# Optimization experiments

Measured on AMD Instinct MI355X. Metric: run time of the kernel, lower is better.

Reference implementation:

```python
import jax, jax.numpy as jnp
import numpy as np

B, F, C, H, W = 16, 256, 64, 64, 64   # batch, features, z_channels(e_dim), height, width
N_E = 512                              # codebooksize
BETA = 1.0
EPS = 1e-5


def setup_inputs() -> dict:
    key = jax.random.key(0)
    ks = jax.random.split(key, 4)
    x = jax.random.normal(ks[0], (B, F, H, W), jnp.float32)
    emb = jax.random.normal(ks[1], (N_E, C), jnp.float32)
    emb = emb / jnp.linalg.norm(emb, axis=1, keepdims=True)  # points on hypersphere
    return dict(
        x=x,
        bn1_gamma=jnp.ones((F,), jnp.float32),
        bn1_beta=jnp.zeros((F,), jnp.float32),
        conv1_w=jax.random.normal(ks[2], (C, F), jnp.float32) * np.float32(1.0 / np.sqrt(F)),
        conv1_b=jnp.zeros((C,), jnp.float32),
        conv2_w=jax.random.normal(ks[3], (C, C), jnp.float32) * np.float32(1.0 / np.sqrt(C)),
        conv2_b=jnp.zeros((C,), jnp.float32),
        embedding=emb,
        r=jnp.ones((N_E,), jnp.float32),
    )


def reference(x, bn1_gamma, bn1_beta, conv1_w, conv1_b, conv2_w, conv2_b, embedding, r):
    sg = jax.lax.stop_gradient
    # BatchNorm2d (training mode: batch stats, biased variance)
    mu = x.mean(axis=(0, 2, 3), keepdims=True)
    var = x.var(axis=(0, 2, 3), keepdims=True)
    x1 = (x - mu) * jax.lax.rsqrt(var + EPS)
    x1 = x1 * bn1_gamma[None, :, None, None] + bn1_beta[None, :, None, None]
    # 1x1 convs (note: original overwrites norm2 output, conv2 consumes conv1 output directly)
    x1 = jnp.einsum('bfhw,cf->bchw', x1, conv1_w) + conv1_b[None, :, None, None]
    z = jnp.einsum('bchw,oc->bohw', x1, conv2_w) + conv2_b[None, :, None, None]

    zf = z.reshape(-1, C)  # [B*C*H*W/e_dim view == flat rows of e_dim]
    # codebook angular statistics (norms detached, as torch.Tensor(list) detaches)
    d1 = embedding @ embedding.T                                 # [n_e, n_e]
    en = sg(jnp.linalg.norm(embedding, axis=1))                  # [n_e]
    edx = jnp.clip(d1 / (en[:, None] * en[None, :]), -0.99999, 0.99999)
    ang = jnp.arccos(edx)
    total_min_distance = jnp.mean(jnp.sort(ang, axis=0)[1])      # kthvalue(.,2,dim=0)
    codebookvariance = jnp.mean(jnp.var(ang, axis=1, ddof=1))    # torch.var unbiased

    # VQ dispatch: squared L2 distances + argmin + gather
    d = (zf ** 2).sum(1, keepdims=True) + (embedding ** 2).sum(1) - 2.0 * (zf @ embedding.T)
    idx = jnp.argmin(d, axis=1)                                  # [ntok]
    z_q = embedding[idx].reshape(z.shape)

    hsw = jnp.mean(jnp.square(r - en))
    # legacy=True path with beta=1.0, ignorezq=False, disentangle=True
    loss = jnp.mean((sg(z_q) - z) ** 2) + BETA * jnp.mean((z_q - sg(z)) ** 2)
    loss = loss + hsw + (codebookvariance - total_min_distance)

    z_q = z + sg(z_q - z)  # straight-through
    cb_loss = jnp.float32(0.0)  # prev_cb is None
    r_c = r + sg(jnp.clip(r, 0.9, 1.1) - r)  # Clamp with straight-through grad
    mean_r = jnp.mean(r_c)
    return (loss, z_q, codebookvariance, total_min_distance, hsw, cb_loss, mean_r)
```

## Files before the change

kernel.cpp:

```cpp
#include <hip/hip_runtime.h>
#include <math.h>


#define CAP    2048
#define MARGIN 4e-3f

#define WS_WHI  0
#define WS_WLO  8192
#define WS_BP   16384
#define WS_EN   16448
#define WS_E2   16960
#define WS_ACC  17472
#define WS_CNT  17480
#define WS_WL   17488
#define WS_EFT  19536
#define WS_WD   52304
#define WS_BPD  85072
#define WS_EHI  85200
#define WS_ELO  101584
#define WS_PART 117968
#define WS_SV   122064
#define WS_SM   122576

typedef __attribute__((ext_vector_type(8))) __bf16 bf16v8;
typedef __attribute__((ext_vector_type(2))) __bf16 bf16v2;
typedef __attribute__((ext_vector_type(4))) float  f32v4;
typedef __attribute__((ext_vector_type(4))) unsigned u32v4;

__device__ __forceinline__ unsigned short f2bf(float f) {
    __bf16 h = (__bf16)f;
    return __builtin_bit_cast(unsigned short, h);
}
__device__ __forceinline__ float bf2f(unsigned short h) {
    union { unsigned u; float f; } v; v.u = ((unsigned)h) << 16; return v.f;
}
__device__ __forceinline__ unsigned pack_bf2(float a, float b) {
    bf16v2 v = { (__bf16)a, (__bf16)b };
    return __builtin_bit_cast(unsigned, v);
}
__device__ __forceinline__ float bfhi(float a) {
    return (float)(__bf16)a;
}
__device__ __forceinline__ void load_lds16(const float* g, unsigned* l) {
    __builtin_amdgcn_global_load_lds((const __attribute__((address_space(1))) void*)g,
                                     (__attribute__((address_space(3))) void*)l, 16, 0, 0);
}

__global__ __launch_bounds__(256) void bn_stats_prep(
    const float* __restrict__ x, double* __restrict__ part,
    const float* __restrict__ emb,
    float* __restrict__ eft, float* __restrict__ en, float* __restrict__ e2,
    unsigned short* __restrict__ ehi, unsigned short* __restrict__ elo,
    float* __restrict__ sv, float* __restrict__ sm)
{
    const int t = threadIdx.x;

    if (blockIdx.x < 1024) {
        const int f = blockIdx.x >> 2, ch = blockIdx.x & 3;
        double s0 = 0.0, s1 = 0.0, q0 = 0.0, q1 = 0.0, q2 = 0.0, q3 = 0.0;
        #pragma unroll
        for (int bb = 0; bb < 4; ++bb) {
            const int b = ch * 4 + bb;
            const float4* p = (const float4*)(x + ((size_t)(b * 256 + f) << 12));
            #pragma unroll
            for (int ii = 0; ii < 4; ++ii) {
                float4 u = p[t + ii * 256];
                double dx = u.x, dy = u.y, dz = u.z, dw = u.w;
                s0 += dx + dy; s1 += dz + dw;
                q0 = fma(dx, dx, q0); q1 = fma(dy, dy, q1);
                q2 = fma(dz, dz, q2); q3 = fma(dw, dw, q3);
            }
        }
        double s = s0 + s1, q = (q0 + q1) + (q2 + q3);
        #pragma unroll
        for (int off = 32; off; off >>= 1) { s += __shfl_xor(s, off, 64); q += __shfl_xor(q, off, 64); }
        __shared__ double sh[8];
        const int wv = t >> 6;
        if ((t & 63) == 0) { sh[wv * 2] = s; sh[wv * 2 + 1] = q; }
        __syncthreads();
        if (t == 0) {
            part[blockIdx.x * 2]     = (sh[0] + sh[2]) + (sh[4] + sh[6]);
            part[blockIdx.x * 2 + 1] = (sh[1] + sh[3]) + (sh[5] + sh[7]);
        }
    } else if (blockIdx.x < 1088) {
        const int blk = blockIdx.x - 1024;
        const int lane = t & 63, wv = t >> 6;
        #pragma unroll
        for (int rr = 0; rr < 2; ++rr) {
            int n = blk * 8 + rr * 4 + wv;
            float v = emb[n * 64 + lane];
            eft[lane * 512 + n] = v;
            unsigned short hb = f2bf(v);
            unsigned short lb = f2bf(v - bf2f(hb));
            int pos = (lane >> 3) ^ (n & 7);
            ehi[n * 64 + pos * 8 + (lane & 7)] = hb;
            elo[n * 64 + pos * 8 + (lane & 7)] = lb;
            float qq = v * v;
            #pragma unroll
            for (int off = 32; off; off >>= 1) qq += __shfl_xor(qq, off, 64);
            if (lane == 0) { e2[n] = qq; en[n] = sqrtf(qq); }
        }
    } else {
        const int i = blockIdx.x - 1088;
        const int lane = t & 63, wv = t >> 6;
        __shared__ float ei_sh[64];
        __shared__ float ang[512];
        if (t < 64) ei_sh[t] = emb[(i << 6) + t];
        __syncthreads();
        float ni0 = 0.f, ni1 = 0.f, ni2 = 0.f, ni3 = 0.f;
        #pragma unroll
        for (int k = 0; k < 64; k += 4) {
            ni0 = fmaf(ei_sh[k + 0], ei_sh[k + 0], ni0);
            ni1 = fmaf(ei_sh[k + 1], ei_sh[k + 1], ni1);
            ni2 = fmaf(ei_sh[k + 2], ei_sh[k + 2], ni2);
            ni3 = fmaf(ei_sh[k + 3], ei_sh[k + 3], ni3);
        }
        const float eni = sqrtf((ni0 + ni1) + (ni2 + ni3));
        #pragma unroll
        for (int jj = 0; jj < 2; ++jj) {
            const int j = t + jj * 256;
            const float4* er = (const float4*)(emb + ((size_t)j << 6));
            float d0 = 0.f, d1 = 0.f, d2 = 0.f, d3 = 0.f;
            float n0 = 0.f, n1 = 0.f, n2 = 0.f, n3 = 0.f;
            #pragma unroll
            for (int k4 = 0; k4 < 16; ++k4) {
                float4 u = er[k4];
                const float* e4 = ei_sh + k4 * 4;
                d0 = fmaf(u.x, e4[0], d0); d1 = fmaf(u.y, e4[1], d1);
                d2 = fmaf(u.z, e4[2], d2); d3 = fmaf(u.w, e4[3], d3);
                n0 = fmaf(u.x, u.x, n0);   n1 = fmaf(u.y, u.y, n1);
                n2 = fmaf(u.z, u.z, n2);   n3 = fmaf(u.w, u.w, n3);
            }
            float dot = (d0 + d1) + (d2 + d3);
            float enj = sqrtf((n0 + n1) + (n2 + n3));
            float xv = dot / (eni * enj);
            xv = fminf(fmaxf(xv, -0.99999f), 0.99999f);
            ang[j] = acosf(xv);
        }
        __syncthreads();
        if (wv == 0) {
            float m1 = 3.4e38f, m2 = 3.4e38f, ssum = 0.f;
            #pragma unroll
            for (int t8 = 0; t8 < 8; ++t8) {
                float a = ang[t8 * 64 + lane];
                ssum += a;
                if (a < m1) { m2 = m1; m1 = a; }
                else if (a < m2) m2 = a;
            }
            #pragma unroll
            for (int off = 32; off; off >>= 1) ssum += __shfl_xor(ssum, off, 64);
            #pragma unroll
            for (int off = 32; off; off >>= 1) {
                float o1 = __shfl_xor(m1, off, 64);
                float o2 = __shfl_xor(m2, off, 64);
                if (o1 < m1) { m2 = fminf(m1, o2); m1 = o1; }
                else          m2 = fminf(m2, o1);
            }
            float mean = ssum * (1.f / 512.f);
            float vs = 0.f;
            #pragma unroll
            for (int t8 = 0; t8 < 8; ++t8) {
                float tt = ang[t8 * 64 + lane] - mean;
                vs = fmaf(tt, tt, vs);
            }
            #pragma unroll
            for (int off = 32; off; off >>= 1) vs += __shfl_xor(vs, off, 64);
            if (lane == 0) { sv[i] = vs * (1.f / 511.f); sm[i] = m2; }
        }
    }
}

__global__ __launch_bounds__(256) void prep(
    const float* __restrict__ w1, const float* __restrict__ w2,
    const float* __restrict__ b1, const float* __restrict__ b2,
    const float* __restrict__ gamma, const float* __restrict__ beta,
    const double* __restrict__ part,
    unsigned short* __restrict__ whi, unsigned short* __restrict__ wlo,
    double* __restrict__ Wd,
    double* __restrict__ bpd, float* __restrict__ bp,
    float* __restrict__ accs, int* __restrict__ cnt)
{
    __shared__ double sh_ad[4];
    __shared__ double cdl[256];
    __shared__ double red[4][64];
    __shared__ double tsh[64];
    const int t = threadIdx.x;

    if (blockIdx.x < 64) {
        const int o = t & 63, fi = t >> 6;
        const int f = blockIdx.x * 4 + fi;
        if (o == 0) {
            double s = (part[(4 * f) * 2]     + part[(4 * f + 1) * 2])
                     + (part[(4 * f + 2) * 2] + part[(4 * f + 3) * 2]);
            double q = (part[(4 * f) * 2 + 1]     + part[(4 * f + 1) * 2 + 1])
                     + (part[(4 * f + 2) * 2 + 1] + part[(4 * f + 3) * 2 + 1]);
            double mean = s * (1.0 / 65536.0);
            double var  = q * (1.0 / 65536.0) - mean * mean;
            sh_ad[fi] = (double)gamma[f] / sqrt(var + 1e-5);
        }
        __syncthreads();
        double s = 0.0;
        for (int c = 0; c < 64; ++c)
            s = fma((double)w2[o * 64 + c], (double)w1[c * 256 + f], s);
        double wp = s * sh_ad[fi];
        Wd[o * 256 + f] = wp;
        {
            float wpf = (float)wp;
            unsigned short wh = f2bf(wpf);
            unsigned short wlv = f2bf(wpf - bf2f(wh));
            int mt = o >> 4, cq_ = o & 15, sK = f >> 5, qd_ = (f >> 3) & 3, j = f & 7;
            int idx = ((mt * 8 + sK) * 64 + qd_ * 16 + cq_) * 8 + j;
            whi[idx] = wh; wlo[idx] = wlv;
        }
    } else {
        {
            const int f = t;
            double s = (part[(4 * f) * 2]     + part[(4 * f + 1) * 2])
                     + (part[(4 * f + 2) * 2] + part[(4 * f + 3) * 2]);
            double q = (part[(4 * f) * 2 + 1]     + part[(4 * f + 1) * 2 + 1])
                     + (part[(4 * f + 2) * 2 + 1] + part[(4 * f + 3) * 2 + 1]);
            double mean = s * (1.0 / 65536.0);
            double var  = q * (1.0 / 65536.0) - mean * mean;
            double a = (double)gamma[f] / sqrt(var + 1e-5);
            cdl[f] = (double)beta[f] - mean * a;
        }
        __syncthreads();
        const int o = t & 63, p = t >> 6;
        double ss = 0.0;
        for (int j = 0; j < 64; ++j) {
            int fidx = p * 64 + j;
            ss = fma((double)w1[o * 256 + fidx], cdl[fidx], ss);
        }
        red[p][o] = ss; __syncthreads();
        if (t < 64) tsh[t] = (double)b1[t] + (red[0][t] + red[1][t]) + (red[2][t] + red[3][t]);
        __syncthreads();
        if (t < 64) {
            double bb = (double)b2[t];
            for (int c = 0; c < 64; ++c)
                bb = fma((double)w2[t * 64 + c], tsh[c], bb);
            bpd[t] = bb;
            bp[t]  = (float)bb;
        }
        if (t < 8) accs[t] = 0.f;
        if (t == 0) cnt[0] = 0;
    }
}

__global__ __launch_bounds__(256, 2) void fused_gemm_vq(
    const float* __restrict__ x,
    const unsigned short* __restrict__ whi,
    const unsigned short* __restrict__ wlo,
    const float* __restrict__ bp,
    const float* __restrict__ emb,
    const float* __restrict__ e2,
    const unsigned short* __restrict__ ehi,
    const unsigned short* __restrict__ elo,
    float* __restrict__ accs,
    int* __restrict__ cnt, int* __restrict__ wl,
    float* __restrict__ zq)
{
    __shared__ __align__(16) unsigned smem[4880];
    enum { OAR = 0,
           OE2 = 4096, OZ2 = 4608, ODT = 4672, OD2T = 4736, OIT = 4800 };
    float* e2s = (float*)(smem + OE2);
    float* z2s = (float*)(smem + OZ2);
    float* dT  = (float*)(smem + ODT);
    float* d2T = (float*)(smem + OD2T);
    int*   iT  = (int*)(smem + OIT);

    const int tid = threadIdx.x, lane = tid & 63, wv = tid >> 6;
    const int wvu = __builtin_amdgcn_readfirstlane(wv);
    const int b = blockIdx.x >> 6, h = blockIdx.x & 63;
    const int cq = lane & 15, qd = lane >> 4;

    bf16v8 Ahi[8], Alo[8];
    #pragma unroll
    for (int s = 0; s < 8; ++s) {
        Ahi[s] = *(const bf16v8*)(whi + ((size_t)((wvu * 8 + s) * 64 + lane)) * 8);
        Alo[s] = *(const bf16v8*)(wlo + ((size_t)((wvu * 8 + s) * 64 + lane)) * 8);
    }
    float bpv[4];
    #pragma unroll
    for (int r = 0; r < 4; ++r) bpv[r] = bp[wvu * 16 + qd * 4 + r];
    e2s[tid]       = e2[tid];
    e2s[tid + 256] = e2[tid + 256];

    const float* xb = x + ((size_t)(b * 256 + wvu * 16) << 12) + (h << 6) + lane;
    float xva[16], xvb[16];
    #pragma unroll
    for (int i = 0; i < 16; ++i) xva[i] = xb[(size_t)i << 12];
    #pragma unroll
    for (int i = 0; i < 16; ++i) xvb[i] = xb[((size_t)(64 + i)) << 12];

    f32v4 acc[4];
    #pragma unroll
    for (int nt = 0; nt < 4; ++nt) acc[nt] = (f32v4){bpv[0], bpv[1], bpv[2], bpv[3]};

#define GEMM_CHUNK(CHK, CUR)                                                          \
    {                                                                                 \
        __syncthreads();                                                 \
        {                                                                             \
            unsigned hb[8], lb[8];                                                    \
            _Pragma("unroll")                                                         \
            for (int p = 0; p < 8; ++p) {                                             \
                float a = CUR[2 * p], bq = CUR[2 * p + 1];                            \
                hb[p] = pack_bf2(a, bq);                                              \
                lb[p] = pack_bf2(a - bfhi(a), bq - bfhi(bq));                         \
            }                                                                         \
            const int b0 = lane * 32 + (((2 * wvu) ^ (lane & 7)) << 2);               \
            const int b1 = lane * 32 + (((2 * wvu + 1) ^ (lane & 7)) << 2);           \
            *(u32v4*)(smem + OAR + b0)        = (u32v4){hb[0], hb[1], hb[2], hb[3]};  \
            *(u32v4*)(smem + OAR + b1)        = (u32v4){hb[4], hb[5], hb[6], hb[7]};  \
            *(u32v4*)(smem + OAR + 2048 + b0) = (u32v4){lb[0], lb[1], lb[2], lb[3]};  \
            *(u32v4*)(smem + OAR + 2048 + b1) = (u32v4){lb[4], lb[5], lb[6], lb[7]};  \
        }                                                                             \
        __syncthreads();                                                \
        if (CHK < 2) {                               \
            const float* xb2 = xb + ((size_t)((CHK + 2) * 64) << 12);                 \
            _Pragma("unroll")                                                         \
            for (int i = 0; i < 16; ++i) CUR[i] = xb2[(size_t)i << 12];               \
        }                                                                             \
        _Pragma("unroll")                                                             \
        for (int st2 = 0; st2 < 2; ++st2) {                                           \
            const int s = CHK * 2 + st2;                                              \
            _Pragma("unroll")                                                         \
            for (int nt = 0; nt < 4; ++nt) {                                          \
                const int row = nt * 16 + cq;                                         \
                const int pos = row * 32 + (((st2 * 4 + qd) ^ (row & 7)) << 2);       \
                bf16v8 bh = *(const bf16v8*)(smem + OAR + pos);                       \
                bf16v8 bl = *(const bf16v8*)(smem + OAR + 2048 + pos);                \
                acc[nt] = __builtin_amdgcn_mfma_f32_16x16x32_bf16(Ahi[s], bh, acc[nt], 0, 0, 0); \
                acc[nt] = __builtin_amdgcn_mfma_f32_16x16x32_bf16(Ahi[s], bl, acc[nt], 0, 0, 0); \
                acc[nt] = __builtin_amdgcn_mfma_f32_16x16x32_bf16(Alo[s], bh, acc[nt], 0, 0, 0); \
            }                                                                         \
        }                                                                             \
    }

    GEMM_CHUNK(0, xva)
    GEMM_CHUNK(1, xvb)
    GEMM_CHUNK(2, xva)
    GEMM_CHUNK(3, xvb)
#undef GEMM_CHUNK

    __syncthreads();

    {
        float z2p[4];
        #pragma unroll
        for (int r = 0; r < 4; ++r) {
            float p2 = 0.f;
            #pragma unroll
            for (int nt = 0; nt < 4; ++nt) p2 = fmaf(acc[nt][r], acc[nt][r], p2);
            #pragma unroll
            for (int off = 1; off <= 8; off <<= 1) p2 += __shfl_xor(p2, off, 64);
            z2p[r] = p2;
        }
        if (cq == 0) {
            #pragma unroll
            for (int r = 0; r < 4; ++r) z2s[wvu * 16 + qd * 4 + r] = z2p[r];
        }
        unsigned short* ar = (unsigned short*)(smem + OAR);
        #pragma unroll
        for (int nt = 0; nt < 4; ++nt) {
            const int w = nt * 16 + cq;
            const int gz = w >> 3, kj = w & 7;
            #pragma unroll
            for (int r = 0; r < 4; ++r) {
                const int tok = wvu * 16 + qd * 4 + r;
                const int hw = tok * 64 + ((gz ^ (tok & 7)) << 3) + kj;
                unsigned short zh = f2bf(acc[nt][r]);
                ar[hw]        = zh;
                ar[4096 + hw] = f2bf(acc[nt][r] - bf2f(zh));
            }
        }
    }
    __syncthreads();

    const int x7 = cq & 7;
    bf16v8 vahi[2], valo[2];
    {
        const int rbase = (wvu * 16 + cq) * 32;
        #pragma unroll
        for (int s = 0; s < 2; ++s) {
            int pos = ((s * 4 + qd) ^ x7) * 4;
            vahi[s] = *(const bf16v8*)(smem + OAR + rbase + pos);
            valo[s] = *(const bf16v8*)(smem + OAR + 2048 + rbase + pos);
        }
    }
    __syncthreads();

    {
        const float* gh = (const float*)ehi;
        const float* gl = (const float*)elo;
        load_lds16(gh + wvu * 256 + lane * 4,        smem + OAR + wvu * 256);
        load_lds16(gl + wvu * 256 + lane * 4,        smem + OAR + 1024 + wvu * 256);
        load_lds16(gh + 1024 + wvu * 256 + lane * 4, smem + OAR + 2048 + wvu * 256);
        load_lds16(gl + 1024 + wvu * 256 + lane * 4, smem + OAR + 3072 + wvu * 256);
    }

    float m1[4] = {-3.4e38f, -3.4e38f, -3.4e38f, -3.4e38f};
    float m2[4] = {-3.4e38f, -3.4e38f, -3.4e38f, -3.4e38f};
    int   i1[4] = {0, 0, 0, 0};
    const int p0 = (qd ^ x7) * 4, p1 = ((4 + qd) ^ x7) * 4;

    #pragma unroll 1
    for (int t2 = 0; t2 < 32; ++t2) {
        if ((t2 & 1) == 0) {
            __syncthreads();
            int st = t2 >> 1;
            if (st >= 1 && st < 15) {
                const float* gh = (const float*)ehi + (size_t)(st + 1) * 1024;
                const float* gl = (const float*)elo + (size_t)(st + 1) * 1024;
                unsigned* dst = smem + OAR + ((st + 1) & 1) * 2048;
                load_lds16(gh + wvu * 256 + lane * 4, dst + wvu * 256);
                load_lds16(gl + wvu * 256 + lane * 4, dst + 1024 + wvu * 256);
            }
        }
        const int rb = OAR + ((t2 >> 1) & 1) * 2048 + ((t2 & 1) * 16 + cq) * 32;
        bf16v8 bh0 = *(const bf16v8*)(smem + rb + p0);
        bf16v8 bh1 = *(const bf16v8*)(smem + rb + p1);
        bf16v8 bl0 = *(const bf16v8*)(smem + rb + 1024 + p0);
        bf16v8 bl1 = *(const bf16v8*)(smem + rb + 1024 + p1);
        const float eps = e2s[t2 * 16 + cq];
        f32v4 a = {0.f, 0.f, 0.f, 0.f};
        __builtin_amdgcn_s_setprio(1);
        a = __builtin_amdgcn_mfma_f32_16x16x32_bf16(vahi[0], bh0, a, 0, 0, 0);
        a = __builtin_amdgcn_mfma_f32_16x16x32_bf16(vahi[1], bh1, a, 0, 0, 0);
        a = __builtin_amdgcn_mfma_f32_16x16x32_bf16(vahi[0], bl0, a, 0, 0, 0);
        a = __builtin_amdgcn_mfma_f32_16x16x32_bf16(vahi[1], bl1, a, 0, 0, 0);
        a = __builtin_amdgcn_mfma_f32_16x16x32_bf16(valo[0], bh0, a, 0, 0, 0);
        a = __builtin_amdgcn_mfma_f32_16x16x32_bf16(valo[1], bh1, a, 0, 0, 0);
        __builtin_amdgcn_s_setprio(0);
        const int n = t2 * 16 + cq;
        #pragma unroll
        for (int r = 0; r < 4; ++r) {
            float s = fmaf(-0.5f, eps, a[r]);
            bool gt = s > m1[r];
            m2[r] = fminf(fmaxf(s, m2[r]), m1[r]);
            i1[r] = gt ? n : i1[r];
            m1[r] = fmaxf(s, m1[r]);
        }
    }

    #pragma unroll
    for (int r = 0; r < 4; ++r) {
        #pragma unroll
        for (int off = 1; off <= 8; off <<= 1) {
            float o1 = __shfl_xor(m1[r], off, 64);
            float o2 = __shfl_xor(m2[r], off, 64);
            int   oi = __shfl_xor(i1[r], off, 64);
            if (o1 > m1[r] || (o1 == m1[r] && oi < i1[r])) {
                m2[r] = fmaxf(m1[r], o2); m1[r] = o1; i1[r] = oi;
            } else {
                m2[r] = fmaxf(m2[r], o1);
            }
        }
    }
    if (cq == 0) {
        #pragma unroll
        for (int r = 0; r < 4; ++r) {
            int tok = wvu * 16 + qd * 4 + r;
            dT[tok] = m1[r]; d2T[tok] = m2[r]; iT[tok] = i1[r];
        }
    }
    __syncthreads();

    if (wv == 0) {
        float s1 = dT[lane], s2 = d2T[lane];
        if (s1 - s2 < MARGIN * 0.5f) {
            int pos = atomicAdd(cnt, 1);
            if (pos < CAP) wl[pos] = ((b << 6) + lane) * 64 + h;
        }
        float ms = z2s[lane] - 2.f * s1;
        #pragma unroll
        for (int off = 32; off; off >>= 1) ms += __shfl_xor(ms, off, 64);
        if (lane == 0) atomicAdd(accs + 0, ms);
    }
    __syncthreads();

    float* zrow = zq + ((size_t)(b * 64) << 12) + (h << 6) + lane;
    #pragma unroll
    for (int cc = 0; cc < 16; ++cc) {
        int c = wvu * 16 + cc;
        int id = iT[c];
        zrow[(size_t)c << 12] = emb[(id << 6) + lane];
    }
}

__global__ __launch_bounds__(256) void refine_fin(
    const float* __restrict__ x,
    const double* __restrict__ Wd,
    const double* __restrict__ bpd,
    const float* __restrict__ emb,
    const float* __restrict__ eft,
    const int* __restrict__ cnt, const int* __restrict__ wl,
    float* __restrict__ zq,
    const float* __restrict__ accs, const float* __restrict__ en,
    const float* __restrict__ sv, const float* __restrict__ sm,
    const float* __restrict__ r, float* __restrict__ out)
{
    const int tid = threadIdx.x, lane = tid & 63, wv = tid >> 6;

    if (blockIdx.x == 2048) {
        if (wv == 0) {
            float hs = 0.f, rs = 0.f, cv = 0.f, tm = 0.f;
            #pragma unroll
            for (int jj = 0; jj < 8; ++jj) {
                int n = (jj << 6) + lane;
                float rv = r[n];
                float d = rv - en[n];
                hs = fmaf(d, d, hs);
                rs += fminf(fmaxf(rv, 0.9f), 1.1f);
                cv += sv[n];
                tm += sm[n];
            }
            #pragma unroll
            for (int off = 32; off; off >>= 1) {
                hs += __shfl_xor(hs, off, 64); rs += __shfl_xor(rs, off, 64);
                cv += __shfl_xor(cv, off, 64); tm += __shfl_xor(tm, off, 64);
            }
            if (lane == 0) {
                float hsw    = hs * (1.f / 512.f);
                float mean_r = rs * (1.f / 512.f);
                float mse    = accs[0] * (1.f / 4194304.f);
                float cbv    = cv * (1.f / 512.f);
                float tmd    = tm * (1.f / 512.f);
                float loss   = 2.f * mse + hsw + (cbv - tmd);
                out[0]       = loss;
                out[4194305] = cbv;
                out[4194306] = tmd;
                out[4194307] = hsw;
                out[4194308] = 0.f;
                out[4194309] = mean_r;
            }
        }
        return;
    }

    int count = cnt[0]; if (count > CAP) count = CAP;
    const int it = blockIdx.x;
    if (it >= count) return;

    __shared__ double zp[4][64];
    __shared__ double zs[64];
    __shared__ double dsh[4];
    __shared__ int    ish[4];

    const int r2 = wl[it];
    const int b = r2 >> 12, c = (r2 >> 6) & 63, h = r2 & 63;

    {
        const float* xp = x + (((size_t)(b * 256 + wv * 64)) << 12) + (h << 6) + lane;
        const double* wrow = Wd + c * 256 + wv * 64;
        double zc0 = 0.0, zc1 = 0.0, zc2 = 0.0, zc3 = 0.0;
        double zc4 = 0.0, zc5 = 0.0, zc6 = 0.0, zc7 = 0.0;
        #pragma unroll
        for (int f = 0; f < 64; f += 8) {
            float a0 = xp[(size_t)(f + 0) << 12];
            float a1 = xp[(size_t)(f + 1) << 12];
            float a2 = xp[(size_t)(f + 2) << 12];
            float a3 = xp[(size_t)(f + 3) << 12];
            float a4 = xp[(size_t)(f + 4) << 12];
            float a5 = xp[(size_t)(f + 5) << 12];
            float a6 = xp[(size_t)(f + 6) << 12];
            float a7 = xp[(size_t)(f + 7) << 12];
            zc0 = fma(wrow[f + 0], (double)a0, zc0);
            zc1 = fma(wrow[f + 1], (double)a1, zc1);
            zc2 = fma(wrow[f + 2], (double)a2, zc2);
            zc3 = fma(wrow[f + 3], (double)a3, zc3);
            zc4 = fma(wrow[f + 4], (double)a4, zc4);
            zc5 = fma(wrow[f + 5], (double)a5, zc5);
            zc6 = fma(wrow[f + 6], (double)a6, zc6);
            zc7 = fma(wrow[f + 7], (double)a7, zc7);
        }
        zp[wv][lane] = ((zc0 + zc1) + (zc2 + zc3)) + ((zc4 + zc5) + (zc6 + zc7));
    }
    __syncthreads();
    if (tid < 64) zs[tid] = (zp[0][tid] + zp[1][tid]) + (zp[2][tid] + zp[3][tid]) + bpd[c];
    __syncthreads();

    const int n0 = tid, n1 = tid + 256;
    double d0a = 0.0, d0b = 0.0, d0c = 0.0, d0d = 0.0;
    double d1a = 0.0, d1b = 0.0, d1c = 0.0, d1d = 0.0;
    #pragma unroll 4
    for (int k = 0; k < 64; k += 4) {
        double z0 = zs[k], z1 = zs[k + 1], z2 = zs[k + 2], z3 = zs[k + 3];
        double t;
        t = z0 - (double)eft[((k + 0) << 9) + n0]; d0a = fma(t, t, d0a);
        t = z1 - (double)eft[((k + 1) << 9) + n0]; d0b = fma(t, t, d0b);
        t = z2 - (double)eft[((k + 2) << 9) + n0]; d0c = fma(t, t, d0c);
        t = z3 - (double)eft[((k + 3) << 9) + n0]; d0d = fma(t, t, d0d);
        t = z0 - (double)eft[((k + 0) << 9) + n1]; d1a = fma(t, t, d1a);
        t = z1 - (double)eft[((k + 1) << 9) + n1]; d1b = fma(t, t, d1b);
        t = z2 - (double)eft[((k + 2) << 9) + n1]; d1c = fma(t, t, d1c);
        t = z3 - (double)eft[((k + 3) << 9) + n1]; d1d = fma(t, t, d1d);
    }
    double d0 = (d0a + d0b) + (d0c + d0d);
    double d1 = (d1a + d1b) + (d1c + d1d);
    double dm; int im;
    if (d1 < d0) { dm = d1; im = n1; } else { dm = d0; im = n0; }

    #pragma unroll
    for (int off = 32; off; off >>= 1) {
        double od = __shfl_xor(dm, off, 64);
        int    oi = __shfl_xor(im, off, 64);
        if (od < dm || (od == dm && oi < im)) { dm = od; im = oi; }
    }
    if (lane == 0) { dsh[wv] = dm; ish[wv] = im; }
    __syncthreads();

    if (tid < 64) {
        double best = dsh[0]; int bi = ish[0];
        #pragma unroll
        for (int wq = 1; wq < 4; ++wq) {
            double od = dsh[wq]; int oi = ish[wq];
            if (od < best || (od == best && oi < bi)) { best = od; bi = oi; }
        }
        zq[((size_t)r2 << 6) + tid] = emb[(bi << 6) + tid];
    }
}

extern "C" void kernel_launch(void* const* d_in, const int* in_sizes, int n_in,
                              void* d_out, int out_size, void* d_ws, size_t ws_size,
                              hipStream_t stream) {
    const float* x   = (const float*)d_in[0];
    const float* g1  = (const float*)d_in[1];
    const float* be1 = (const float*)d_in[2];
    const float* w1  = (const float*)d_in[3];
    const float* b1  = (const float*)d_in[4];
    const float* w2  = (const float*)d_in[5];
    const float* b2  = (const float*)d_in[6];
    const float* emb = (const float*)d_in[7];
    const float* r   = (const float*)d_in[8];
    float* ws = (float*)d_ws;
    float* out = (float*)d_out;

    double* WD   = (double*)(ws + WS_WD);
    double* BPD  = (double*)(ws + WS_BPD);
    double* PART = (double*)(ws + WS_PART);
    int*    CNT  = (int*)(ws + WS_CNT);
    int*    WL   = (int*)(ws + WS_WL);
    unsigned short* WHI = (unsigned short*)(ws + WS_WHI);
    unsigned short* WLO = (unsigned short*)(ws + WS_WLO);
    unsigned short* EHI = (unsigned short*)(ws + WS_EHI);
    unsigned short* ELO = (unsigned short*)(ws + WS_ELO);

    bn_stats_prep<<<1600, 256, 0, stream>>>(x, PART, emb,
                                            ws + WS_EFT, ws + WS_EN, ws + WS_E2,
                                            EHI, ELO, ws + WS_SV, ws + WS_SM);
    prep<<<65, 256, 0, stream>>>(w1, w2, b1, b2, g1, be1, PART,
                                 WHI, WLO, WD, BPD, ws + WS_BP,
                                 ws + WS_ACC, CNT);
    fused_gemm_vq<<<1024, 256, 0, stream>>>(x, WHI, WLO, ws + WS_BP,
                                            emb, ws + WS_E2,
                                            EHI, ELO, ws + WS_ACC, CNT, WL, out + 1);
    refine_fin<<<2049, 256, 0, stream>>>(x, WD, BPD, emb, ws + WS_EFT, CNT, WL,
                                         out + 1, ws + WS_ACC, ws + WS_EN,
                                         ws + WS_SV, ws + WS_SM, r, out);
}
```

Baseline: 183.8 us.

## Fuse four kernels into one persistent kernel with global barriers

```diff
diff --git a/kernel.cpp b/kernel.cpp
--- a/kernel.cpp
+++ b/kernel.cpp
@@ -4,6 +4,7 @@
 
 #define CAP    2048
 #define MARGIN 4e-3f
+#define NBLK   512
 
 #define WS_WHI  0
 #define WS_WLO  8192
@@ -21,6 +22,7 @@
 #define WS_PART 117968
 #define WS_SV   122064
 #define WS_SM   122576
+#define WS_BAR  123088
 
 typedef __attribute__((ext_vector_type(8))) __bf16 bf16v8;
 typedef __attribute__((ext_vector_type(2))) __bf16 bf16v2;
@@ -46,21 +48,43 @@
                                      (__attribute__((address_space(3))) void*)l, 16, 0, 0);
 }
 
-__global__ __launch_bounds__(256) void bn_stats_prep(
-    const float* __restrict__ x, double* __restrict__ part,
-    const float* __restrict__ emb,
-    float* __restrict__ eft, float* __restrict__ en, float* __restrict__ e2,
+__device__ __forceinline__ void gbar(int* bar, int target) {
+    __syncthreads();
+    if (threadIdx.x == 0) {
+        __threadfence();
+        atomicAdd(bar, 1);
+        while (__hip_atomic_load(bar, __ATOMIC_RELAXED, __HIP_MEMORY_SCOPE_AGENT) < target)
+            __builtin_amdgcn_s_sleep(2);
+        __threadfence();
+    }
+    __syncthreads();
+}
+
+__global__ __launch_bounds__(256, 2) void mega(
+    const float* __restrict__ x,
+    const float* __restrict__ w1, const float* __restrict__ w2,
+    const float* __restrict__ b1, const float* __restrict__ b2,
+    const float* __restrict__ gamma, const float* __restrict__ beta,
+    const float* __restrict__ emb, const float* __restrict__ r,
+    unsigned short* __restrict__ whi, unsigned short* __restrict__ wlo,
+    float* __restrict__ bp, float* __restrict__ en, float* __restrict__ e2,
+    float* __restrict__ accs, int* __restrict__ cnt, int* __restrict__ wl,
+    float* __restrict__ eft, double* __restrict__ Wd, double* __restrict__ bpd,
+    double* __restrict__ part,
     unsigned short* __restrict__ ehi, unsigned short* __restrict__ elo,
-    float* __restrict__ sv, float* __restrict__ sm)
+    float* __restrict__ sv, float* __restrict__ sm,
+    int* __restrict__ bar, float* __restrict__ out, float* __restrict__ zq)
 {
-    const int t = threadIdx.x;
-
-    if (blockIdx.x < 1024) {
-        const int f = blockIdx.x >> 2, ch = blockIdx.x & 3;
+    __shared__ __align__(16) unsigned smem[4880];
+    const int t = threadIdx.x, lane = t & 63, wv = t >> 6;
+    const int bid = blockIdx.x;
+
+    {
+        const int f = bid >> 1, ch = bid & 1;
         double s0 = 0.0, s1 = 0.0, q0 = 0.0, q1 = 0.0, q2 = 0.0, q3 = 0.0;
-        #pragma unroll
-        for (int bb = 0; bb < 4; ++bb) {
-            const int b = ch * 4 + bb;
+        #pragma unroll 2
+        for (int bb = 0; bb < 8; ++bb) {
+            const int b = ch * 8 + bb;
             const float4* p = (const float4*)(x + ((size_t)(b * 256 + f) << 12));
             #pragma unroll
             for (int ii = 0; ii < 4; ++ii) {
@@ -74,165 +98,142 @@
         double s = s0 + s1, q = (q0 + q1) + (q2 + q3);
         #pragma unroll
         for (int off = 32; off; off >>= 1) { s += __shfl_xor(s, off, 64); q += __shfl_xor(q, off, 64); }
-        __shared__ double sh[8];
-        const int wv = t >> 6;
-        if ((t & 63) == 0) { sh[wv * 2] = s; sh[wv * 2 + 1] = q; }
+        double* shd = (double*)smem;
+        if (lane == 0) { shd[wv * 2] = s; shd[wv * 2 + 1] = q; }
         __syncthreads();
         if (t == 0) {
-            part[blockIdx.x * 2]     = (sh[0] + sh[2]) + (sh[4] + sh[6]);
-            part[blockIdx.x * 2 + 1] = (sh[1] + sh[3]) + (sh[5] + sh[7]);
-        }
-    } else if (blockIdx.x < 1088) {
-        const int blk = blockIdx.x - 1024;
-        const int lane = t & 63, wv = t >> 6;
-        #pragma unroll
-        for (int rr = 0; rr < 2; ++rr) {
-            int n = blk * 8 + rr * 4 + wv;
-            float v = emb[n * 64 + lane];
-            eft[lane * 512 + n] = v;
-            unsigned short hb = f2bf(v);
-            unsigned short lb = f2bf(v - bf2f(hb));
-            int pos = (lane >> 3) ^ (n & 7);
-            ehi[n * 64 + pos * 8 + (lane & 7)] = hb;
-            elo[n * 64 + pos * 8 + (lane & 7)] = lb;
-            float qq = v * v;
-            #pragma unroll
-            for (int off = 32; off; off >>= 1) qq += __shfl_xor(qq, off, 64);
-            if (lane == 0) { e2[n] = qq; en[n] = sqrtf(qq); }
-        }
-    } else {
-        const int i = blockIdx.x - 1088;
-        const int lane = t & 63, wv = t >> 6;
-        __shared__ float ei_sh[64];
-        __shared__ float ang[512];
-        if (t < 64) ei_sh[t] = emb[(i << 6) + t];
-        __syncthreads();
-        float ni0 = 0.f, ni1 = 0.f, ni2 = 0.f, ni3 = 0.f;
-        #pragma unroll
-        for (int k = 0; k < 64; k += 4) {
-            ni0 = fmaf(ei_sh[k + 0], ei_sh[k + 0], ni0);
-            ni1 = fmaf(ei_sh[k + 1], ei_sh[k + 1], ni1);
-            ni2 = fmaf(ei_sh[k + 2], ei_sh[k + 2], ni2);
-            ni3 = fmaf(ei_sh[k + 3], ei_sh[k + 3], ni3);
-        }
-        const float eni = sqrtf((ni0 + ni1) + (ni2 + ni3));
-        #pragma unroll
-        for (int jj = 0; jj < 2; ++jj) {
-            const int j = t + jj * 256;
-            const float4* er = (const float4*)(emb + ((size_t)j << 6));
-            float d0 = 0.f, d1 = 0.f, d2 = 0.f, d3 = 0.f;
-            float n0 = 0.f, n1 = 0.f, n2 = 0.f, n3 = 0.f;
-            #pragma unroll
-            for (int k4 = 0; k4 < 16; ++k4) {
-                float4 u = er[k4];
-                const float* e4 = ei_sh + k4 * 4;
-                d0 = fmaf(u.x, e4[0], d0); d1 = fmaf(u.y, e4[1], d1);
-                d2 = fmaf(u.z, e4[2], d2); d3 = fmaf(u.w, e4[3], d3);
-                n0 = fmaf(u.x, u.x, n0);   n1 = fmaf(u.y, u.y, n1);
-                n2 = fmaf(u.z, u.z, n2);   n3 = fmaf(u.w, u.w, n3);
-            }
-            float dot = (d0 + d1) + (d2 + d3);
-            float enj = sqrtf((n0 + n1) + (n2 + n3));
-            float xv = dot / (eni * enj);
-            xv = fminf(fmaxf(xv, -0.99999f), 0.99999f);
-            ang[j] = acosf(xv);
-        }
-        __syncthreads();
-        if (wv == 0) {
-            float m1 = 3.4e38f, m2 = 3.4e38f, ssum = 0.f;
-            #pragma unroll
-            for (int t8 = 0; t8 < 8; ++t8) {
-                float a = ang[t8 * 64 + lane];
-                ssum += a;
-                if (a < m1) { m2 = m1; m1 = a; }
-                else if (a < m2) m2 = a;
-            }
-            #pragma unroll
-            for (int off = 32; off; off >>= 1) ssum += __shfl_xor(ssum, off, 64);
-            #pragma unroll
-            for (int off = 32; off; off >>= 1) {
-                float o1 = __shfl_xor(m1, off, 64);
-                float o2 = __shfl_xor(m2, off, 64);
-                if (o1 < m1) { m2 = fminf(m1, o2); m1 = o1; }
-                else          m2 = fminf(m2, o1);
-            }
-            float mean = ssum * (1.f / 512.f);
-            float vs = 0.f;
-            #pragma unroll
-            for (int t8 = 0; t8 < 8; ++t8) {
-                float tt = ang[t8 * 64 + lane] - mean;
-                vs = fmaf(tt, tt, vs);
-            }
-            #pragma unroll
-            for (int off = 32; off; off >>= 1) vs += __shfl_xor(vs, off, 64);
-            if (lane == 0) { sv[i] = vs * (1.f / 511.f); sm[i] = m2; }
+            part[bid * 2]     = (shd[0] + shd[2]) + (shd[4] + shd[6]);
+            part[bid * 2 + 1] = (shd[1] + shd[3]) + (shd[5] + shd[7]);
+        }
+
+        if (bid >= 448) {
+            const int blk = bid - 448;
+            #pragma unroll
+            for (int rr = 0; rr < 2; ++rr) {
+                int n = blk * 8 + rr * 4 + wv;
+                float v = emb[n * 64 + lane];
+                eft[lane * 512 + n] = v;
+                unsigned short hb = f2bf(v);
+                unsigned short lb = f2bf(v - bf2f(hb));
+                int pos = (lane >> 3) ^ (n & 7);
+                ehi[n * 64 + pos * 8 + (lane & 7)] = hb;
+                elo[n * 64 + pos * 8 + (lane & 7)] = lb;
+                float qq = v * v;
+                #pragma unroll
+                for (int off = 32; off; off >>= 1) qq += __shfl_xor(qq, off, 64);
+                if (lane == 0) { e2[n] = qq; en[n] = sqrtf(qq); }
+            }
+        }
+
+        {
+            const int i = bid;
+            float* ei_sh = (float*)(smem + 64);
+            float* ang   = (float*)(smem + 128);
+            if (t < 64) ei_sh[t] = emb[(i << 6) + t];
+            __syncthreads();
+            float ni0 = 0.f, ni1 = 0.f, ni2 = 0.f, ni3 = 0.f;
+            #pragma unroll
+            for (int k = 0; k < 64; k += 4) {
+                ni0 = fmaf(ei_sh[k + 0], ei_sh[k + 0], ni0);
+                ni1 = fmaf(ei_sh[k + 1], ei_sh[k + 1], ni1);
+                ni2 = fmaf(ei_sh[k + 2], ei_sh[k + 2], ni2);
+                ni3 = fmaf(ei_sh[k + 3], ei_sh[k + 3], ni3);
+            }
+            const float eni = sqrtf((ni0 + ni1) + (ni2 + ni3));
+            #pragma unroll
+            for (int jj = 0; jj < 2; ++jj) {
+                const int j = t + jj * 256;
+                const float4* er = (const float4*)(emb + ((size_t)j << 6));
+                float d0 = 0.f, d1 = 0.f, d2 = 0.f, d3 = 0.f;
+                float n0 = 0.f, n1 = 0.f, n2 = 0.f, n3 = 0.f;
+                #pragma unroll
+                for (int k4 = 0; k4 < 16; ++k4) {
+                    float4 u = er[k4];
+                    const float* e4 = ei_sh + k4 * 4;
+                    d0 = fmaf(u.x, e4[0], d0); d1 = fmaf(u.y, e4[1], d1);
+                    d2 = fmaf(u.z, e4[2], d2); d3 = fmaf(u.w, e4[3], d3);
+                    n0 = fmaf(u.x, u.x, n0);   n1 = fmaf(u.y, u.y, n1);
+                    n2 = fmaf(u.z, u.z, n2);   n3 = fmaf(u.w, u.w, n3);
+                }
+                float dot = (d0 + d1) + (d2 + d3);
+                float enj = sqrtf((n0 + n1) + (n2 + n3));
+                float xv = dot / (eni * enj);
+                xv = fminf(fmaxf(xv, -0.99999f), 0.99999f);
+                ang[j] = acosf(xv);
+            }
+            __syncthreads();
+            if (wv == 0) {
+                float m1 = 3.4e38f, m2 = 3.4e38f, ssum = 0.f;
+                #pragma unroll
+                for (int t8 = 0; t8 < 8; ++t8) {
+                    float a = ang[t8 * 64 + lane];
+                    ssum += a;
+                    if (a < m1) { m2 = m1; m1 = a; }
+                    else if (a < m2) m2 = a;
+                }
+                #pragma unroll
+                for (int off = 32; off; off >>= 1) ssum += __shfl_xor(ssum, off, 64);
+                #pragma unroll
+                for (int off = 32; off; off >>= 1) {
+                    float o1 = __shfl_xor(m1, off, 64);
+                    float o2 = __shfl_xor(m2, off, 64);
+                    if (o1 < m1) { m2 = fminf(m1, o2); m1 = o1; }
+                    else          m2 = fminf(m2, o1);
+                }
+                float mean = ssum * (1.f / 512.f);
+                float vs = 0.f;
+                #pragma unroll
+                for (int t8 = 0; t8 < 8; ++t8) {
+                    float tt = ang[t8 * 64 + lane] - mean;
+                    vs = fmaf(tt, tt, vs);
+                }
+                #pragma unroll
+                for (int off = 32; off; off >>= 1) vs += __shfl_xor(vs, off, 64);
+                if (lane == 0) { sv[i] = vs * (1.f / 511.f); sm[i] = m2; }
+            }
         }
     }
-}
-
-__global__ __launch_bounds__(256) void prep(
-    const float* __restrict__ w1, const float* __restrict__ w2,
-    const float* __restrict__ b1, const float* __restrict__ b2,
-    const float* __restrict__ gamma, const float* __restrict__ beta,
-    const double* __restrict__ part,
-    unsigned short* __restrict__ whi, unsigned short* __restrict__ wlo,
-    double* __restrict__ Wd,
-    double* __restrict__ bpd, float* __restrict__ bp,
-    float* __restrict__ accs, int* __restrict__ cnt)
-{
-    __shared__ double sh_ad[4];
-    __shared__ double cdl[256];
-    __shared__ double red[4][64];
-    __shared__ double tsh[64];
-    const int t = threadIdx.x;
-
-    if (blockIdx.x < 64) {
-        const int o = t & 63, fi = t >> 6;
-        const int f = blockIdx.x * 4 + fi;
-        if (o == 0) {
-            double s = (part[(4 * f) * 2]     + part[(4 * f + 1) * 2])
-                     + (part[(4 * f + 2) * 2] + part[(4 * f + 3) * 2]);
-            double q = (part[(4 * f) * 2 + 1]     + part[(4 * f + 1) * 2 + 1])
-                     + (part[(4 * f + 2) * 2 + 1] + part[(4 * f + 3) * 2 + 1]);
+
+    gbar(bar, NBLK);
+
+    if (bid < 64) {
+        const int o = bid, f = t;
+        double s = part[(2 * f) * 2]     + part[(2 * f + 1) * 2];
+        double q = part[(2 * f) * 2 + 1] + part[(2 * f + 1) * 2 + 1];
+        double mean = s * (1.0 / 65536.0);
+        double var  = q * (1.0 / 65536.0) - mean * mean;
+        double af = (double)gamma[f] / sqrt(var + 1e-5);
+        double a = 0.0;
+        for (int c = 0; c < 64; ++c)
+            a = fma((double)w2[o * 64 + c], (double)w1[c * 256 + f], a);
+        double wp = a * af;
+        Wd[o * 256 + f] = wp;
+        float wpf = (float)wp;
+        unsigned short wh = f2bf(wpf);
+        unsigned short wlv = f2bf(wpf - bf2f(wh));
+        int mt = o >> 4, cq_ = o & 15, sK = f >> 5, qd_ = (f >> 3) & 3, j = f & 7;
+        int idx = ((mt * 8 + sK) * 64 + qd_ * 16 + cq_) * 8 + j;
+        whi[idx] = wh; wlo[idx] = wlv;
+    } else if (bid == 64) {
+        double* cdl = (double*)smem;
+        double* red = cdl + 256;
+        double* tsh = red + 256;
+        {
+            const int f = t;
+            double s = part[(2 * f) * 2]     + part[(2 * f + 1) * 2];
+            double q = part[(2 * f) * 2 + 1] + part[(2 * f + 1) * 2 + 1];
             double mean = s * (1.0 / 65536.0);
             double var  = q * (1.0 / 65536.0) - mean * mean;
-            sh_ad[fi] = (double)gamma[f] / sqrt(var + 1e-5);
-        }
-        __syncthreads();
-        double s = 0.0;
-        for (int c = 0; c < 64; ++c)
-            s = fma((double)w2[o * 64 + c], (double)w1[c * 256 + f], s);
-        double wp = s * sh_ad[fi];
-        Wd[o * 256 + f] = wp;
-        {
-            float wpf = (float)wp;
-            unsigned short wh = f2bf(wpf);
-            unsigned short wlv = f2bf(wpf - bf2f(wh));
-            int mt = o >> 4, cq_ = o & 15, sK = f >> 5, qd_ = (f >> 3) & 3, j = f & 7;
-            int idx = ((mt * 8 + sK) * 64 + qd_ * 16 + cq_) * 8 + j;
-            whi[idx] = wh; wlo[idx] = wlv;
-        }
-    } else {
-        {
-            const int f = t;
-            double s = (part[(4 * f) * 2]     + part[(4 * f + 1) * 2])
-                     + (part[(4 * f + 2) * 2] + part[(4 * f + 3) * 2]);
-            double q = (part[(4 * f) * 2 + 1]     + part[(4 * f + 1) * 2 + 1])
-                     + (part[(4 * f + 2) * 2 + 1] + part[(4 * f + 3) * 2 + 1]);
-            double mean = s * (1.0 / 65536.0);
-            double var  = q * (1.0 / 65536.0) - mean * mean;
-            double a = (double)gamma[f] / sqrt(var + 1e-5);
-            cdl[f] = (double)beta[f] - mean * a;
+            double af = (double)gamma[f] / sqrt(var + 1e-5);
+            cdl[f] = (double)beta[f] - mean * af;
         }
         __syncthreads();
         const int o = t & 63, p = t >> 6;
         double ss = 0.0;
-        for (int j = 0; j < 64; ++j) {
-            int fidx = p * 64 + j;
-            ss = fma((double)w1[o * 256 + fidx], cdl[fidx], ss);
-        }
-        red[p][o] = ss; __syncthreads();
-        if (t < 64) tsh[t] = (double)b1[t] + (red[0][t] + red[1][t]) + (red[2][t] + red[3][t]);
+        for (int j = 0; j < 64; ++j)
+            ss = fma((double)w1[o * 256 + p * 64 + j], cdl[p * 64 + j], ss);
+        red[p * 64 + o] = ss; __syncthreads();
+        if (t < 64) tsh[t] = (double)b1[t] + (red[t] + red[64 + t]) + (red[128 + t] + red[192 + t]);
         __syncthreads();
         if (t < 64) {
             double bb = (double)b2[t];
@@ -244,57 +245,48 @@
         if (t < 8) accs[t] = 0.f;
         if (t == 0) cnt[0] = 0;
     }
-}
-
-__global__ __launch_bounds__(256, 2) void fused_gemm_vq(
-    const float* __restrict__ x,
-    const unsigned short* __restrict__ whi,
-    const unsigned short* __restrict__ wlo,
-    const float* __restrict__ bp,
-    const float* __restrict__ emb,
-    const float* __restrict__ e2,
-    const unsigned short* __restrict__ ehi,
-    const unsigned short* __restrict__ elo,
-    float* __restrict__ accs,
-    int* __restrict__ cnt, int* __restrict__ wl,
-    float* __restrict__ zq)
-{
-    __shared__ __align__(16) unsigned smem[4880];
-    enum { OAR = 0,
-           OE2 = 4096, OZ2 = 4608, ODT = 4672, OD2T = 4736, OIT = 4800 };
-    float* e2s = (float*)(smem + OE2);
-    float* z2s = (float*)(smem + OZ2);
-    float* dT  = (float*)(smem + ODT);
-    float* d2T = (float*)(smem + OD2T);
-    int*   iT  = (int*)(smem + OIT);
-
-    const int tid = threadIdx.x, lane = tid & 63, wv = tid >> 6;
-    const int wvu = __builtin_amdgcn_readfirstlane(wv);
-    const int b = blockIdx.x >> 6, h = blockIdx.x & 63;
-    const int cq = lane & 15, qd = lane >> 4;
-
-    bf16v8 Ahi[8], Alo[8];
-    #pragma unroll
-    for (int s = 0; s < 8; ++s) {
-        Ahi[s] = *(const bf16v8*)(whi + ((size_t)((wvu * 8 + s) * 64 + lane)) * 8);
-        Alo[s] = *(const bf16v8*)(wlo + ((size_t)((wvu * 8 + s) * 64 + lane)) * 8);
-    }
-    float bpv[4];
-    #pragma unroll
-    for (int r = 0; r < 4; ++r) bpv[r] = bp[wvu * 16 + qd * 4 + r];
-    e2s[tid]       = e2[tid];
-    e2s[tid + 256] = e2[tid + 256];
-
-    const float* xb = x + ((size_t)(b * 256 + wvu * 16) << 12) + (h << 6) + lane;
-    float xva[16], xvb[16];
-    #pragma unroll
-    for (int i = 0; i < 16; ++i) xva[i] = xb[(size_t)i << 12];
-    #pragma unroll
-    for (int i = 0; i < 16; ++i) xvb[i] = xb[((size_t)(64 + i)) << 12];
-
-    f32v4 acc[4];
-    #pragma unroll
-    for (int nt = 0; nt < 4; ++nt) acc[nt] = (f32v4){bpv[0], bpv[1], bpv[2], bpv[3]};
+
+    gbar(bar, 2 * NBLK);
+
+    {
+        enum { OAR = 0, OE2 = 4096, OZ2 = 4608, ODT = 4672, OD2T = 4736, OIT = 4800 };
+        float* e2s = (float*)(smem + OE2);
+        float* z2s = (float*)(smem + OZ2);
+        float* dT  = (float*)(smem + ODT);
+        float* d2T = (float*)(smem + OD2T);
+        int*   iT  = (int*)(smem + OIT);
+
+        const int tid = t;
+        const int wvu = __builtin_amdgcn_readfirstlane(wv);
+        const int cq = lane & 15, qd = lane >> 4;
+
+        bf16v8 Ahi[8], Alo[8];
+        #pragma unroll
+        for (int s = 0; s < 8; ++s) {
+            Ahi[s] = *(const bf16v8*)(whi + ((size_t)((wvu * 8 + s) * 64 + lane)) * 8);
+            Alo[s] = *(const bf16v8*)(wlo + ((size_t)((wvu * 8 + s) * 64 + lane)) * 8);
+        }
+        float bpv[4];
+        #pragma unroll
+        for (int rr = 0; rr < 4; ++rr) bpv[rr] = bp[wvu * 16 + qd * 4 + rr];
+        e2s[tid]       = e2[tid];
+        e2s[tid + 256] = e2[tid + 256];
+
+        #pragma unroll 1
+        for (int tok = 0; tok < 2; ++tok) {
+            const int idx = bid * 2 + tok;
+            const int b = idx >> 6, h = idx & 63;
+
+            const float* xb = x + ((size_t)(b * 256 + wvu * 16) << 12) + (h << 6) + lane;
+            float xva[16], xvb[16];
+            #pragma unroll
+            for (int i = 0; i < 16; ++i) xva[i] = xb[(size_t)i << 12];
+            #pragma unroll
+            for (int i = 0; i < 16; ++i) xvb[i] = xb[((size_t)(64 + i)) << 12];
+
+            f32v4 acc[4];
+            #pragma unroll
+            for (int nt = 0; nt < 4; ++nt) acc[nt] = (f32v4){bpv[0], bpv[1], bpv[2], bpv[3]};
 
 #define GEMM_CHUNK(CHK, CUR)                                                          \
     {                                                                                 \
@@ -315,7 +307,7 @@
             *(u32v4*)(smem + OAR + 2048 + b1) = (u32v4){lb[4], lb[5], lb[6], lb[7]};  \
         }                                                                             \
         __syncthreads();                                                \
-        if (CHK < 2) {                               \
+        if (CHK < 2) {                                                                \
             const float* xb2 = xb + ((size_t)((CHK + 2) * 64) << 12);                 \
             _Pragma("unroll")                                                         \
             for (int i = 0; i < 16; ++i) CUR[i] = xb2[(size_t)i << 12];               \
@@ -336,287 +328,275 @@
         }                                                                             \
     }
 
-    GEMM_CHUNK(0, xva)
-    GEMM_CHUNK(1, xvb)
-    GEMM_CHUNK(2, xva)
-    GEMM_CHUNK(3, xvb)
+            GEMM_CHUNK(0, xva)
+            GEMM_CHUNK(1, xvb)
+            GEMM_CHUNK(2, xva)
+            GEMM_CHUNK(3, xvb)
 #undef GEMM_CHUNK
 
-    __syncthreads();
+            __syncthreads();
+
+            {
+                float z2p[4];
+                #pragma unroll
+                for (int rr = 0; rr < 4; ++rr) {
+                    float p2 = 0.f;
+                    #pragma unroll
+                    for (int nt = 0; nt < 4; ++nt) p2 = fmaf(acc[nt][rr], acc[nt][rr], p2);
+                    #pragma unroll
+                    for (int off = 1; off <= 8; off <<= 1) p2 += __shfl_xor(p2, off, 64);
+                    z2p[rr] = p2;
+                }
+                if (cq == 0) {
+                    #pragma unroll
+                    for (int rr = 0; rr < 4; ++rr) z2s[wvu * 16 + qd * 4 + rr] = z2p[rr];
+                }
+                unsigned short* ar = (unsigned short*)(smem + OAR);
+                #pragma unroll
+                for (int nt = 0; nt < 4; ++nt) {
+                    const int w = nt * 16 + cq;
+                    const int gz = w >> 3, kj = w & 7;
+                    #pragma unroll
+                    for (int rr = 0; rr < 4; ++rr) {
+                        const int tk = wvu * 16 + qd * 4 + rr;
+                        const int hw = tk * 64 + ((gz ^ (tk & 7)) << 3) + kj;
+                        unsigned short zh = f2bf(acc[nt][rr]);
+                        ar[hw]        = zh;
+                        ar[4096 + hw] = f2bf(acc[nt][rr] - bf2f(zh));
+                    }
+                }
+            }
+            __syncthreads();
+
+            const int x7 = cq & 7;
+            bf16v8 vahi[2], valo[2];
+            {
+                const int rbase = (wvu * 16 + cq) * 32;
+                #pragma unroll
+                for (int s = 0; s < 2; ++s) {
+                    int pos = ((s * 4 + qd) ^ x7) * 4;
+                    vahi[s] = *(const bf16v8*)(smem + OAR + rbase + pos);
+                    valo[s] = *(const bf16v8*)(smem + OAR + 2048 + rbase + pos);
+                }
+            }
+            __syncthreads();
+
+            {
+                const float* gh = (const float*)ehi;
+                const float* gl = (const float*)elo;
+                load_lds16(gh + wvu * 256 + lane * 4,        smem + OAR + wvu * 256);
+                load_lds16(gl + wvu * 256 + lane * 4,        smem + OAR + 1024 + wvu * 256);
+                load_lds16(gh + 1024 + wvu * 256 + lane * 4, smem + OAR + 2048 + wvu * 256);
+                load_lds16(gl + 1024 + wvu * 256 + lane * 4, smem + OAR + 3072 + wvu * 256);
+            }
+
+            float m1[4] = {-3.4e38f, -3.4e38f, -3.4e38f, -3.4e38f};
+            float m2[4] = {-3.4e38f, -3.4e38f, -3.4e38f, -3.4e38f};
+            int   i1[4] = {0, 0, 0, 0};
+            const int p0 = (qd ^ x7) * 4, p1 = ((4 + qd) ^ x7) * 4;
+
+            #pragma unroll 1
+            for (int t2 = 0; t2 < 32; ++t2) {
+                if ((t2 & 1) == 0) {
+                    __syncthreads();
+                    int st = t2 >> 1;
+                    if (st >= 1 && st < 15) {
+                        const float* gh = (const float*)ehi + (size_t)(st + 1) * 1024;
+                        const float* gl = (const float*)elo + (size_t)(st + 1) * 1024;
+                        unsigned* dst = smem + OAR + ((st + 1) & 1) * 2048;
+                        load_lds16(gh + wvu * 256 + lane * 4, dst + wvu * 256);
+                        load_lds16(gl + wvu * 256 + lane * 4, dst + 1024 + wvu * 256);
+                    }
+                }
+                const int rb = OAR + ((t2 >> 1) & 1) * 2048 + ((t2 & 1) * 16 + cq) * 32;
+                bf16v8 bh0 = *(const bf16v8*)(smem + rb + p0);
+                bf16v8 bh1 = *(const bf16v8*)(smem + rb + p1);
+                bf16v8 bl0 = *(const bf16v8*)(smem + rb + 1024 + p0);
+                bf16v8 bl1 = *(const bf16v8*)(smem + rb + 1024 + p1);
+                const float eps = e2s[t2 * 16 + cq];
+                f32v4 a = {0.f, 0.f, 0.f, 0.f};
+                __builtin_amdgcn_s_setprio(1);
+                a = __builtin_amdgcn_mfma_f32_16x16x32_bf16(vahi[0], bh0, a, 0, 0, 0);
+                a = __builtin_amdgcn_mfma_f32_16x16x32_bf16(vahi[1], bh1, a, 0, 0, 0);
+                a = __builtin_amdgcn_mfma_f32_16x16x32_bf16(vahi[0], bl0, a, 0, 0, 0);
+                a = __builtin_amdgcn_mfma_f32_16x16x32_bf16(vahi[1], bl1, a, 0, 0, 0);
+                a = __builtin_amdgcn_mfma_f32_16x16x32_bf16(valo[0], bh0, a, 0, 0, 0);
+                a = __builtin_amdgcn_mfma_f32_16x16x32_bf16(valo[1], bh1, a, 0, 0, 0);
+                __builtin_amdgcn_s_setprio(0);
+                const int n = t2 * 16 + cq;
+                #pragma unroll
+                for (int rr = 0; rr < 4; ++rr) {
+                    float s = fmaf(-0.5f, eps, a[rr]);
+                    bool gt = s > m1[rr];
+                    m2[rr] = fminf(fmaxf(s, m2[rr]), m1[rr]);
+                    i1[rr] = gt ? n : i1[rr];
+                    m1[rr] = fmaxf(s, m1[rr]);
+                }
+            }
+
+            #pragma unroll
+            for (int rr = 0; rr < 4; ++rr) {
+                #pragma unroll
+                for (int off = 1; off <= 8; off <<= 1) {
+                    float o1 = __shfl_xor(m1[rr], off, 64);
+                    float o2 = __shfl_xor(m2[rr], off, 64);
+                    int   oi = __shfl_xor(i1[rr], off, 64);
+                    if (o1 > m1[rr] || (o1 == m1[rr] && oi < i1[rr])) {
+                        m2[rr] = fmaxf(m1[rr], o2); m1[rr] = o1; i1[rr] = oi;
+                    } else {
+                        m2[rr] = fmaxf(m2[rr], o1);
+                    }
+                }
+            }
+            if (cq == 0) {
+                #pragma unroll
+                for (int rr = 0; rr < 4; ++rr) {
+                    int tk = wvu * 16 + qd * 4 + rr;
+                    dT[tk] = m1[rr]; d2T[tk] = m2[rr]; iT[tk] = i1[rr];
+                }
+            }
+            __syncthreads();
+
+            if (wv == 0) {
+                float s1 = dT[lane], s2 = d2T[lane];
+                if (s1 - s2 < MARGIN * 0.5f) {
+                    int pos = atomicAdd(cnt, 1);
+                    if (pos < CAP) wl[pos] = ((b << 6) + lane) * 64 + h;
+                }
+                float ms = z2s[lane] - 2.f * s1;
+                #pragma unroll
+                for (int off = 32; off; off >>= 1) ms += __shfl_xor(ms, off, 64);
+                if (lane == 0) atomicAdd(accs + 0, ms);
+            }
+            __syncthreads();
+
+            float* zrow = zq + ((size_t)(b * 64) << 12) + (h << 6) + lane;
+            #pragma unroll
+            for (int cc = 0; cc < 16; ++cc) {
+                int c = wvu * 16 + cc;
+                int id = iT[c];
+                zrow[(size_t)c << 12] = emb[(id << 6) + lane];
+            }
+        }
+    }
+
+    gbar(bar, 3 * NBLK);
+
+    if (bid == 0 && wv == 0) {
+        float hs = 0.f, rs = 0.f, cv = 0.f, tm = 0.f;
+        #pragma unroll
+        for (int jj = 0; jj < 8; ++jj) {
+            int n = (jj << 6) + lane;
+            float rv = r[n];
+            float d = rv - en[n];
+            hs = fmaf(d, d, hs);
+            rs += fminf(fmaxf(rv, 0.9f), 1.1f);
+            cv += sv[n];
+            tm += sm[n];
+        }
+        #pragma unroll
+        for (int off = 32; off; off >>= 1) {
+            hs += __shfl_xor(hs, off, 64); rs += __shfl_xor(rs, off, 64);
+            cv += __shfl_xor(cv, off, 64); tm += __shfl_xor(tm, off, 64);
+        }
+        if (lane == 0) {
+            float hsw    = hs * (1.f / 512.f);
+            float mean_r = rs * (1.f / 512.f);
+            float mse    = accs[0] * (1.f / 4194304.f);
+            float cbv    = cv * (1.f / 512.f);
+            float tmd    = tm * (1.f / 512.f);
+            float loss   = 2.f * mse + hsw + (cbv - tmd);
+            out[0]       = loss;
+            out[4194305] = cbv;
+            out[4194306] = tmd;
+            out[4194307] = hsw;
+            out[4194308] = 0.f;
+            out[4194309] = mean_r;
+        }
+    }
 
     {
-        float z2p[4];
-        #pragma unroll
-        for (int r = 0; r < 4; ++r) {
-            float p2 = 0.f;
-            #pragma unroll
-            for (int nt = 0; nt < 4; ++nt) p2 = fmaf(acc[nt][r], acc[nt][r], p2);
-            #pragma unroll
-            for (int off = 1; off <= 8; off <<= 1) p2 += __shfl_xor(p2, off, 64);
-            z2p[r] = p2;
-        }
-        if (cq == 0) {
-            #pragma unroll
-            for (int r = 0; r < 4; ++r) z2s[wvu * 16 + qd * 4 + r] = z2p[r];
-        }
-        unsigned short* ar = (unsigned short*)(smem + OAR);
-        #pragma unroll
-        for (int nt = 0; nt < 4; ++nt) {
-            const int w = nt * 16 + cq;
-            const int gz = w >> 3, kj = w & 7;
-            #pragma unroll
-            for (int r = 0; r < 4; ++r) {
-                const int tok = wvu * 16 + qd * 4 + r;
-                const int hw = tok * 64 + ((gz ^ (tok & 7)) << 3) + kj;
-                unsigned short zh = f2bf(acc[nt][r]);
-                ar[hw]        = zh;
-                ar[4096 + hw] = f2bf(acc[nt][r] - bf2f(zh));
-            }
-        }
-    }
-    __syncthreads();
-
-    const int x7 = cq & 7;
-    bf16v8 vahi[2], valo[2];
-    {
-        const int rbase = (wvu * 16 + cq) * 32;
-        #pragma unroll
-        for (int s = 0; s < 2; ++s) {
-            int pos = ((s * 4 + qd) ^ x7) * 4;
-            vahi[s] = *(const bf16v8*)(smem + OAR + rbase + pos);
-            valo[s] = *(const bf16v8*)(smem + OAR + 2048 + rbase + pos);
-        }
-    }
-    __syncthreads();
-
-    {
-        const float* gh = (const float*)ehi;
-        const float* gl = (const float*)elo;
-        load_lds16(gh + wvu * 256 + lane * 4,        smem + OAR + wvu * 256);
-        load_lds16(gl + wvu * 256 + lane * 4,        smem + OAR + 1024 + wvu * 256);
-        load_lds16(gh + 1024 + wvu * 256 + lane * 4, smem + OAR + 2048 + wvu * 256);
-        load_lds16(gl + 1024 + wvu * 256 + lane * 4, smem + OAR + 3072 + wvu * 256);
-    }
-
-    float m1[4] = {-3.4e38f, -3.4e38f, -3.4e38f, -3.4e38f};
-    float m2[4] = {-3.4e38f, -3.4e38f, -3.4e38f, -3.4e38f};
-    int   i1[4] = {0, 0, 0, 0};
-    const int p0 = (qd ^ x7) * 4, p1 = ((4 + qd) ^ x7) * 4;
-
-    #pragma unroll 1
-    for (int t2 = 0; t2 < 32; ++t2) {
-        if ((t2 & 1) == 0) {
-            __syncthreads();
-            int st = t2 >> 1;
-            if (st >= 1 && st < 15) {
-                const float* gh = (const float*)ehi + (size_t)(st + 1) * 1024;
-                const float* gl = (const float*)elo + (size_t)(st + 1) * 1024;
-                unsigned* dst = smem + OAR + ((st + 1) & 1) * 2048;
-                load_lds16(gh + wvu * 256 + lane * 4, dst + wvu * 256);
-                load_lds16(gl + wvu * 256 + lane * 4, dst + 1024 + wvu * 256);
-            }
-        }
-        const int rb = OAR + ((t2 >> 1) & 1) * 2048 + ((t2 & 1) * 16 + cq) * 32;
-        bf16v8 bh0 = *(const bf16v8*)(smem + rb + p0);
-        bf16v8 bh1 = *(const bf16v8*)(smem + rb + p1);
-        bf16v8 bl0 = *(const bf16v8*)(smem + rb + 1024 + p0);
-        bf16v8 bl1 = *(const bf16v8*)(smem + rb + 1024 + p1);
-        const float eps = e2s[t2 * 16 + cq];
-        f32v4 a = {0.f, 0.f, 0.f, 0.f};
-        __builtin_amdgcn_s_setprio(1);
-        a = __builtin_amdgcn_mfma_f32_16x16x32_bf16(vahi[0], bh0, a, 0, 0, 0);
-        a = __builtin_amdgcn_mfma_f32_16x16x32_bf16(vahi[1], bh1, a, 0, 0, 0);
-        a = __builtin_amdgcn_mfma_f32_16x16x32_bf16(vahi[0], bl0, a, 0, 0, 0);
-        a = __builtin_amdgcn_mfma_f32_16x16x32_bf16(vahi[1], bl1, a, 0, 0, 0);
-        a = __builtin_amdgcn_mfma_f32_16x16x32_bf16(valo[0], bh0, a, 0, 0, 0);
-        a = __builtin_amdgcn_mfma_f32_16x16x32_bf16(valo[1], bh1, a, 0, 0, 0);
-        __builtin_amdgcn_s_setprio(0);
-        const int n = t2 * 16 + cq;
-        #pragma unroll
-        for (int r = 0; r < 4; ++r) {
-            float s = fmaf(-0.5f, eps, a[r]);
-            bool gt = s > m1[r];
-            m2[r] = fminf(fmaxf(s, m2[r]), m1[r]);
-            i1[r] = gt ? n : i1[r];
-            m1[r] = fmaxf(s, m1[r]);
-        }
-    }
-
-    #pragma unroll
-    for (int r = 0; r < 4; ++r) {
-        #pragma unroll
-        for (int off = 1; off <= 8; off <<= 1) {
-            float o1 = __shfl_xor(m1[r], off, 64);
-            float o2 = __shfl_xor(m2[r], off, 64);
-            int   oi = __shfl_xor(i1[r], off, 64);
-            if (o1 > m1[r] || (o1 == m1[r] && oi < i1[r])) {
-                m2[r] = fmaxf(m1[r], o2); m1[r] = o1; i1[r] = oi;
-            } else {
-                m2[r] = fmaxf(m2[r], o1);
-            }
-        }
-    }
-    if (cq == 0) {
-        #pragma unroll
-        for (int r = 0; r < 4; ++r) {
-            int tok = wvu * 16 + qd * 4 + r;
-            dT[tok] = m1[r]; d2T[tok] = m2[r]; iT[tok] = i1[r];
-        }
-    }
-    __syncthreads();
-
-    if (wv == 0) {
-        float s1 = dT[lane], s2 = d2T[lane];
-        if (s1 - s2 < MARGIN * 0.5f) {
-            int pos = atomicAdd(cnt, 1);
-            if (pos < CAP) wl[pos] = ((b << 6) + lane) * 64 + h;
-        }
-        float ms = z2s[lane] - 2.f * s1;
-        #pragma unroll
-        for (int off = 32; off; off >>= 1) ms += __shfl_xor(ms, off, 64);
-        if (lane == 0) atomicAdd(accs + 0, ms);
-    }
-    __syncthreads();
-
-    float* zrow = zq + ((size_t)(b * 64) << 12) + (h << 6) + lane;
-    #pragma unroll
-    for (int cc = 0; cc < 16; ++cc) {
-        int c = wvu * 16 + cc;
-        int id = iT[c];
-        zrow[(size_t)c << 12] = emb[(id << 6) + lane];
-    }
-}
-
-__global__ __launch_bounds__(256) void refine_fin(
-    const float* __restrict__ x,
-    const double* __restrict__ Wd,
-    const double* __restrict__ bpd,
-    const float* __restrict__ emb,
-    const float* __restrict__ eft,
-    const int* __restrict__ cnt, const int* __restrict__ wl,
-    float* __restrict__ zq,
-    const float* __restrict__ accs, const float* __restrict__ en,
-    const float* __restrict__ sv, const float* __restrict__ sm,
-    const float* __restrict__ r, float* __restrict__ out)
-{
-    const int tid = threadIdx.x, lane = tid & 63, wv = tid >> 6;
-
-    if (blockIdx.x == 2048) {
-        if (wv == 0) {
-            float hs = 0.f, rs = 0.f, cv = 0.f, tm = 0.f;
-            #pragma unroll
-            for (int jj = 0; jj < 8; ++jj) {
-                int n = (jj << 6) + lane;
-                float rv = r[n];
-                float d = rv - en[n];
-                hs = fmaf(d, d, hs);
-                rs += fminf(fmaxf(rv, 0.9f), 1.1f);
-                cv += sv[n];
-                tm += sm[n];
-            }
+        int count = cnt[0]; if (count > CAP) count = CAP;
+        double* zp   = (double*)smem;
+        double* zs   = zp + 256;
+        double* dshd = zs + 64;
+        int*    ishd = (int*)(dshd + 4);
+
+        for (int it = bid; it < count; it += NBLK) {
+            const int r2 = wl[it];
+            const int b = r2 >> 12, c = (r2 >> 6) & 63, h = r2 & 63;
+
+            {
+                const float* xp = x + (((size_t)(b * 256 + wv * 64)) << 12) + (h << 6) + lane;
+                const double* wrow = Wd + c * 256 + wv * 64;
+                double zc0 = 0.0, zc1 = 0.0, zc2 = 0.0, zc3 = 0.0;
+                double zc4 = 0.0, zc5 = 0.0, zc6 = 0.0, zc7 = 0.0;
+                #pragma unroll
+                for (int f = 0; f < 64; f += 8) {
+                    float a0 = xp[(size_t)(f + 0) << 12];
+                    float a1 = xp[(size_t)(f + 1) << 12];
+                    float a2 = xp[(size_t)(f + 2) << 12];
+                    float a3 = xp[(size_t)(f + 3) << 12];
+                    float a4 = xp[(size_t)(f + 4) << 12];
+                    float a5 = xp[(size_t)(f + 5) << 12];
+                    float a6 = xp[(size_t)(f + 6) << 12];
+                    float a7 = xp[(size_t)(f + 7) << 12];
+                    zc0 = fma(wrow[f + 0], (double)a0, zc0);
+                    zc1 = fma(wrow[f + 1], (double)a1, zc1);
+                    zc2 = fma(wrow[f + 2], (double)a2, zc2);
+                    zc3 = fma(wrow[f + 3], (double)a3, zc3);
+                    zc4 = fma(wrow[f + 4], (double)a4, zc4);
+                    zc5 = fma(wrow[f + 5], (double)a5, zc5);
+                    zc6 = fma(wrow[f + 6], (double)a6, zc6);
+                    zc7 = fma(wrow[f + 7], (double)a7, zc7);
+                }
+                zp[wv * 64 + lane] = ((zc0 + zc1) + (zc2 + zc3)) + ((zc4 + zc5) + (zc6 + zc7));
+            }
+            __syncthreads();
+            if (t < 64) zs[t] = (zp[t] + zp[64 + t]) + (zp[128 + t] + zp[192 + t]) + bpd[c];
+            __syncthreads();
+
+            const int n0 = t, n1 = t + 256;
+            double d0a = 0.0, d0b = 0.0, d0c = 0.0, d0d = 0.0;
+            double d1a = 0.0, d1b = 0.0, d1c = 0.0, d1d = 0.0;
+            #pragma unroll 4
+            for (int k = 0; k < 64; k += 4) {
+                double z0 = zs[k], z1 = zs[k + 1], z2 = zs[k + 2], z3 = zs[k + 3];
+                double tt;
+                tt = z0 - (double)eft[((k + 0) << 9) + n0]; d0a = fma(tt, tt, d0a);
+                tt = z1 - (double)eft[((k + 1) << 9) + n0]; d0b = fma(tt, tt, d0b);
+                tt = z2 - (double)eft[((k + 2) << 9) + n0]; d0c = fma(tt, tt, d0c);
+                tt = z3 - (double)eft[((k + 3) << 9) + n0]; d0d = fma(tt, tt, d0d);
+                tt = z0 - (double)eft[((k + 0) << 9) + n1]; d1a = fma(tt, tt, d1a);
+                tt = z1 - (double)eft[((k + 1) << 9) + n1]; d1b = fma(tt, tt, d1b);
+                tt = z2 - (double)eft[((k + 2) << 9) + n1]; d1c = fma(tt, tt, d1c);
+                tt = z3 - (double)eft[((k + 3) << 9) + n1]; d1d = fma(tt, tt, d1d);
+            }
+            double d0 = (d0a + d0b) + (d0c + d0d);
+            double d1 = (d1a + d1b) + (d1c + d1d);
+            double dm; int im;
+            if (d1 < d0) { dm = d1; im = n1; } else { dm = d0; im = n0; }
+
             #pragma unroll
             for (int off = 32; off; off >>= 1) {
-                hs += __shfl_xor(hs, off, 64); rs += __shfl_xor(rs, off, 64);
-                cv += __shfl_xor(cv, off, 64); tm += __shfl_xor(tm, off, 64);
-            }
-            if (lane == 0) {
-                float hsw    = hs * (1.f / 512.f);
-                float mean_r = rs * (1.f / 512.f);
-                float mse    = accs[0] * (1.f / 4194304.f);
-                float cbv    = cv * (1.f / 512.f);
-                float tmd    = tm * (1.f / 512.f);
-                float loss   = 2.f * mse + hsw + (cbv - tmd);
-                out[0]       = loss;
-                out[4194305] = cbv;
-                out[4194306] = tmd;
-                out[4194307] = hsw;
-                out[4194308] = 0.f;
-                out[4194309] = mean_r;
-            }
-        }
-        return;
-    }
-
-    int count = cnt[0]; if (count > CAP) count = CAP;
-    const int it = blockIdx.x;
-    if (it >= count) return;
-
-    __shared__ double zp[4][64];
-    __shared__ double zs[64];
-    __shared__ double dsh[4];
-    __shared__ int    ish[4];
-
-    const int r2 = wl[it];
-    const int b = r2 >> 12, c = (r2 >> 6) & 63, h = r2 & 63;
-
-    {
-        const float* xp = x + (((size_t)(b * 256 + wv * 64)) << 12) + (h << 6) + lane;
-        const double* wrow = Wd + c * 256 + wv * 64;
-        double zc0 = 0.0, zc1 = 0.0, zc2 = 0.0, zc3 = 0.0;
-        double zc4 = 0.0, zc5 = 0.0, zc6 = 0.0, zc7 = 0.0;
-        #pragma unroll
-        for (int f = 0; f < 64; f += 8) {
-            float a0 = xp[(size_t)(f + 0) << 12];
-            float a1 = xp[(size_t)(f + 1) << 12];
-            float a2 = xp[(size_t)(f + 2) << 12];
-            float a3 = xp[(size_t)(f + 3) << 12];
-            float a4 = xp[(size_t)(f + 4) << 12];
-            float a5 = xp[(size_t)(f + 5) << 12];
-            float a6 = xp[(size_t)(f + 6) << 12];
-            float a7 = xp[(size_t)(f + 7) << 12];
-            zc0 = fma(wrow[f + 0], (double)a0, zc0);
-            zc1 = fma(wrow[f + 1], (double)a1, zc1);
-            zc2 = fma(wrow[f + 2], (double)a2, zc2);
-            zc3 = fma(wrow[f + 3], (double)a3, zc3);
-            zc4 = fma(wrow[f + 4], (double)a4, zc4);
-            zc5 = fma(wrow[f + 5], (double)a5, zc5);
-            zc6 = fma(wrow[f + 6], (double)a6, zc6);
-            zc7 = fma(wrow[f + 7], (double)a7, zc7);
-        }
-        zp[wv][lane] = ((zc0 + zc1) + (zc2 + zc3)) + ((zc4 + zc5) + (zc6 + zc7));
-    }
-    __syncthreads();
-    if (tid < 64) zs[tid] = (zp[0][tid] + zp[1][tid]) + (zp[2][tid] + zp[3][tid]) + bpd[c];
-    __syncthreads();
-
-    const int n0 = tid, n1 = tid + 256;
-    double d0a = 0.0, d0b = 0.0, d0c = 0.0, d0d = 0.0;
-    double d1a = 0.0, d1b = 0.0, d1c = 0.0, d1d = 0.0;
-    #pragma unroll 4
-    for (int k = 0; k < 64; k += 4) {
-        double z0 = zs[k], z1 = zs[k + 1], z2 = zs[k + 2], z3 = zs[k + 3];
-        double t;
-        t = z0 - (double)eft[((k + 0) << 9) + n0]; d0a = fma(t, t, d0a);
-        t = z1 - (double)eft[((k + 1) << 9) + n0]; d0b = fma(t, t, d0b);
-        t = z2 - (double)eft[((k + 2) << 9) + n0]; d0c = fma(t, t, d0c);
-        t = z3 - (double)eft[((k + 3) << 9) + n0]; d0d = fma(t, t, d0d);
-        t = z0 - (double)eft[((k + 0) << 9) + n1]; d1a = fma(t, t, d1a);
-        t = z1 - (double)eft[((k + 1) << 9) + n1]; d1b = fma(t, t, d1b);
-        t = z2 - (double)eft[((k + 2) << 9) + n1]; d1c = fma(t, t, d1c);
-        t = z3 - (double)eft[((k + 3) << 9) + n1]; d1d = fma(t, t, d1d);
-    }
-    double d0 = (d0a + d0b) + (d0c + d0d);
-    double d1 = (d1a + d1b) + (d1c + d1d);
-    double dm; int im;
-    if (d1 < d0) { dm = d1; im = n1; } else { dm = d0; im = n0; }
-
-    #pragma unroll
-    for (int off = 32; off; off >>= 1) {
-        double od = __shfl_xor(dm, off, 64);
-        int    oi = __shfl_xor(im, off, 64);
-        if (od < dm || (od == dm && oi < im)) { dm = od; im = oi; }
-    }
-    if (lane == 0) { dsh[wv] = dm; ish[wv] = im; }
-    __syncthreads();
-
-    if (tid < 64) {
-        double best = dsh[0]; int bi = ish[0];
-        #pragma unroll
-        for (int wq = 1; wq < 4; ++wq) {
-            double od = dsh[wq]; int oi = ish[wq];
-            if (od < best || (od == best && oi < bi)) { best = od; bi = oi; }
-        }
-        zq[((size_t)r2 << 6) + tid] = emb[(bi << 6) + tid];
+                double od = __shfl_xor(dm, off, 64);
+                int    oi = __shfl_xor(im, off, 64);
+                if (od < dm || (od == dm && oi < im)) { dm = od; im = oi; }
+            }
+            if (lane == 0) { dshd[wv] = dm; ishd[wv] = im; }
+            __syncthreads();
+
+            if (t < 64) {
+                double best = dshd[0]; int bi = ishd[0];
+                #pragma unroll
+                for (int wq = 1; wq < 4; ++wq) {
+                    double od = dshd[wq]; int oi = ishd[wq];
+                    if (od < best || (od == best && oi < bi)) { best = od; bi = oi; }
+                }
+                zq[((size_t)r2 << 6) + t] = emb[(bi << 6) + t];
+            }
+            __syncthreads();
+        }
     }
 }
 
@@ -640,21 +620,17 @@
     double* PART = (double*)(ws + WS_PART);
     int*    CNT  = (int*)(ws + WS_CNT);
     int*    WL   = (int*)(ws + WS_WL);
+    int*    BAR  = (int*)(ws + WS_BAR);
     unsigned short* WHI = (unsigned short*)(ws + WS_WHI);
     unsigned short* WLO = (unsigned short*)(ws + WS_WLO);
     unsigned short* EHI = (unsigned short*)(ws + WS_EHI);
     unsigned short* ELO = (unsigned short*)(ws + WS_ELO);
 
-    bn_stats_prep<<<1600, 256, 0, stream>>>(x, PART, emb,
-                                            ws + WS_EFT, ws + WS_EN, ws + WS_E2,
-                                            EHI, ELO, ws + WS_SV, ws + WS_SM);
-    prep<<<65, 256, 0, stream>>>(w1, w2, b1, b2, g1, be1, PART,
-                                 WHI, WLO, WD, BPD, ws + WS_BP,
-                                 ws + WS_ACC, CNT);
-    fused_gemm_vq<<<1024, 256, 0, stream>>>(x, WHI, WLO, ws + WS_BP,
-                                            emb, ws + WS_E2,
-                                            EHI, ELO, ws + WS_ACC, CNT, WL, out + 1);
-    refine_fin<<<2049, 256, 0, stream>>>(x, WD, BPD, emb, ws + WS_EFT, CNT, WL,
-                                         out + 1, ws + WS_ACC, ws + WS_EN,
-                                         ws + WS_SV, ws + WS_SM, r, out);
-}
+    hipMemsetAsync(BAR, 0, 4, stream);
+    mega<<<NBLK, 256, 0, stream>>>(x, w1, w2, b1, b2, g1, be1, emb, r,
+                                   WHI, WLO, ws + WS_BP, ws + WS_EN, ws + WS_E2,
+                                   ws + WS_ACC, CNT, WL,
+                                   ws + WS_EFT, WD, BPD, PART,
+                                   EHI, ELO, ws + WS_SV, ws + WS_SM,
+                                   BAR, out, out + 1);
+}
```

Measured after the change: 322.4 us. 75.4% more time.
